# Performance work log

Hardware: AMD Instinct MI355X
Metric: run time of the kernel (lower is better)

The kernel has to match this reference:

```python
import jax, jax.numpy as jnp
import numpy as np

NUM_LEVELS = 16
LEVEL_DIM = 2
LOG2_HASHMAP = 19
TABLE_SIZE = 1 << LOG2_HASHMAP
BASE_RES = 16
PER_LEVEL_SCALE = 2.0
N_QUERIES = 1 << 20

# spatial hashing primes (instant-NGP / Minkowski-style coordinate hash)
_PRIMES = jnp.array([1, 2654435761, 805459861], dtype=jnp.uint32)
# 8 trilinear corner offsets [8,3]
_OFFS = jnp.array([[i, j, k] for i in (0, 1) for j in (0, 1) for k in (0, 1)], dtype=jnp.int32)


def setup_inputs() -> dict:
    key = jax.random.key(0)
    k1, k2 = jax.random.split(key)
    inputs = jax.random.uniform(k1, (N_QUERIES, 3), dtype=jnp.float32, minval=-1.0, maxval=1.0)
    embeddings = jax.random.normal(k2, (NUM_LEVELS, TABLE_SIZE, LEVEL_DIM), dtype=jnp.float32) * 1e-2
    return {"inputs": inputs, "embeddings": embeddings, "bound": 1}


def _encode(inputs, embeddings, bound):
    # channel permutation as in the torch forward: inputs[..., [2, 0, 1]]
    x = inputs[..., jnp.array([2, 0, 1])]
    u = (x / bound + 1.0) * 0.5  # normalize to [0, 1], [N,3]
    resolutions = jnp.asarray(
        np.floor(BASE_RES * PER_LEVEL_SCALE ** np.arange(NUM_LEVELS)), dtype=jnp.float32
    )

    def level_lookup(_, level):
        emb, res = level  # emb [T,F], res scalar
        pos = u * res - 0.5  # align_corners=False
        pos0 = jnp.floor(pos)
        frac = pos - pos0  # [N,3]
        corners = pos0.astype(jnp.int32)[:, None, :] + _OFFS[None]  # [N,8,3]
        cu = corners.astype(jnp.uint32)
        h = (cu[..., 0] * _PRIMES[0]) ^ (cu[..., 1] * _PRIMES[1]) ^ (cu[..., 2] * _PRIMES[2])
        idx = (h & jnp.uint32(TABLE_SIZE - 1)).astype(jnp.int32)  # [N,8]
        feats = emb[idx]  # [N,8,F] gather into sparse grid hash map
        w = jnp.prod(
            jnp.where(_OFFS[None].astype(bool), frac[:, None, :], 1.0 - frac[:, None, :]),
            axis=-1,
        )  # [N,8] trilinear weights
        return None, jnp.sum(feats * w[..., None], axis=1)  # [N,F]

    _, per_level = jax.lax.scan(level_lookup, None, (embeddings, resolutions))  # [L,N,F]
    N = inputs.shape[0]
    # concat per-level features along last dim (level-major), matching torch.cat
    return jnp.moveaxis(per_level, 0, 1).reshape(N, NUM_LEVELS * LEVEL_DIM)


def reference(inputs, embeddings, bound):
    return _encode(inputs, embeddings, float(bound))
```

## Files before the change

### kernel.cpp

```cpp
#include <hip/hip_runtime.h>
#include <hip/hip_fp16.h>

#define NUM_LEVELS 16
#define LOG2_HASHMAP 19
#define TABLE_SIZE (1u << LOG2_HASHMAP)
#define HASH_MASK (TABLE_SIZE - 1u)
#define BASE_RES 16
#define N_QUERIES (1 << 20)
#define BLK 256
#define BLOCKS_PER_LEVEL (N_QUERIES / BLK)

__device__ __forceinline__ float decode_bound(const void* p) {
    int iv = *(const int*)p;
    float fv = __int_as_float(iv);
    float afv = fabsf(fv);
    if (afv >= 1e-8f && afv <= 1e8f) return fv;
    return (float)iv;
}

template <bool USE_WS>
__global__ __launch_bounds__(BLK, 8)
void gather_kernel(const float* __restrict__ in,
                   const float* __restrict__ emb,
                   const void*  __restrict__ bound_ptr,
                   float* __restrict__ dst)
{
    const unsigned P1 = 2654435761u, P2 = 805459861u;
    const int level = blockIdx.x / BLOCKS_PER_LEVEL;
    const int chunk = blockIdx.x % BLOCKS_PER_LEVEL;
    const int n = chunk * BLK + threadIdx.x;

    const float bound = decode_bound(bound_ptr);

    float i0 = in[(size_t)n * 3 + 0];
    float i1 = in[(size_t)n * 3 + 1];
    float i2 = in[(size_t)n * 3 + 2];

    float u0 = __fmul_rn(__fadd_rn(__fdiv_rn(i2, bound), 1.0f), 0.5f);
    float u1 = __fmul_rn(__fadd_rn(__fdiv_rn(i0, bound), 1.0f), 0.5f);
    float u2 = __fmul_rn(__fadd_rn(__fdiv_rn(i1, bound), 1.0f), 0.5f);

    float res = (float)(BASE_RES << level);

    float p0 = __fadd_rn(__fmul_rn(u0, res), -0.5f);
    float p1 = __fadd_rn(__fmul_rn(u1, res), -0.5f);
    float p2 = __fadd_rn(__fmul_rn(u2, res), -0.5f);
    float g0 = floorf(p0), g1 = floorf(p1), g2 = floorf(p2);
    float fr0 = __fsub_rn(p0, g0), fr1 = __fsub_rn(p1, g1), fr2 = __fsub_rn(p2, g2);
    int c0 = (int)g0, c1 = (int)g1, c2 = (int)g2;

    unsigned b0  = (unsigned)c0;
    unsigned b0p = b0 + 1u;
    unsigned b1  = (unsigned)c1 * P1;
    unsigned b1p = b1 + P1;
    unsigned b2  = (unsigned)c2 * P2;
    unsigned b2p = b2 + P2;

    const float2* tbl  = (const float2*)emb + (size_t)level * TABLE_SIZE;
    const float4* tbl4 = (const float4*)tbl;

    unsigned X[4];
    X[0] = b1  ^ b2;
    X[1] = b1  ^ b2p;
    X[2] = b1p ^ b2;
    X[3] = b1p ^ b2p;

    const bool odd = (b0 & 1u) != 0u;

    unsigned E0[4];
    float4 v4[4];
    #pragma unroll
    for (int m = 0; m < 4; ++m) {
        E0[m] = (b0 ^ X[m]) & HASH_MASK;
        v4[m] = tbl4[E0[m] >> 1];
    }

    float2 fb[4] = {make_float2(0.f,0.f), make_float2(0.f,0.f),
                    make_float2(0.f,0.f), make_float2(0.f,0.f)};
    if (odd) {
        #pragma unroll
        for (int m = 0; m < 4; ++m)
            fb[m] = tbl[(b0p ^ X[m]) & HASH_MASK];
    }

    float2 f[8];
    #pragma unroll
    for (int m = 0; m < 4; ++m) {
        bool hi = (E0[m] & 1u) != 0u;
        float2 lo2 = make_float2(v4[m].x, v4[m].y);
        float2 hi2 = make_float2(v4[m].z, v4[m].w);
        f[m]     = hi ? hi2 : lo2;
        f[4 + m] = odd ? fb[m] : (hi ? lo2 : hi2);
    }

    float wx[2] = {1.0f - fr0, fr0};
    float wy[2] = {1.0f - fr1, fr1};
    float wz[2] = {1.0f - fr2, fr2};

    float a0 = 0.0f, a1 = 0.0f;
    #pragma unroll
    for (int c = 0; c < 8; ++c) {
        float w = wx[(c >> 2) & 1] * wy[(c >> 1) & 1] * wz[c & 1];
        a0 += f[c].x * w;
        a1 += f[c].y * w;
    }

    if (USE_WS) {
        __half2 h = __floats2half2_rn(a0, a1);
        union { __half2 h; unsigned u; } cv; cv.h = h;
        unsigned* o = (unsigned*)dst + (size_t)level * N_QUERIES + n;
        *o = cv.u;
    } else {
        float2* o = (float2*)(dst + (size_t)n * 32 + 2 * level);
        *o = make_float2(a0, a1);
    }
}

__global__ __launch_bounds__(BLK, 4)
void transpose_kernel(const unsigned* __restrict__ ws, float* __restrict__ out)
{
    __shared__ unsigned s[NUM_LEVELS][BLK + 1];
    const int n0 = blockIdx.x * BLK;

    #pragma unroll
    for (int l = 0; l < NUM_LEVELS; ++l) {
        s[l][threadIdx.x] = ws[(size_t)l * N_QUERIES + n0 + threadIdx.x];
    }
    __syncthreads();

    float4* o = (float4*)out + (size_t)n0 * 8;
    #pragma unroll
    for (int r = 0; r < 8; ++r) {
        int t = r * BLK + (int)threadIdx.x;
        int n = t >> 3;
        int q = t & 7;
        union { unsigned u; __half2 h; } ca, cb;
        ca.u = s[2 * q][n];
        cb.u = s[2 * q + 1][n];
        float2 a = __half22float2(ca.h);
        float2 b = __half22float2(cb.h);
        o[t] = make_float4(a.x, a.y, b.x, b.y);
    }
}

extern "C" void kernel_launch(void* const* d_in, const int* in_sizes, int n_in,
                              void* d_out, int out_size, void* d_ws, size_t ws_size,
                              hipStream_t stream) {
    const float* in   = (const float*)d_in[0];
    const float* emb  = (const float*)d_in[1];
    const void*  bptr = d_in[2];
    float* out = (float*)d_out;

    const size_t need = (size_t)N_QUERIES * NUM_LEVELS * sizeof(unsigned);
    dim3 block(BLK);
    dim3 ggrid(NUM_LEVELS * BLOCKS_PER_LEVEL);

    if (ws_size >= need) {
        float* ws = (float*)d_ws;
        gather_kernel<true><<<ggrid, block, 0, stream>>>(in, emb, bptr, ws);
        transpose_kernel<<<N_QUERIES / BLK, block, 0, stream>>>((const unsigned*)ws, out);
    } else {
        gather_kernel<false><<<ggrid, block, 0, stream>>>(in, emb, bptr, out);
    }
}
```

Measured before the change: 623.6 us.

## Fuse per-level gather and transpose into one kernel looping over levels

Replaces the level-major gather kernel plus shared-memory transpose with a single kernel where each thread loops over all 16 levels and stages half-precision results in shared memory before writing the interleaved output. This removes the workspace round trip and the second launch. In exchange, the concurrently accessed embedding working set grows from one level's table to all levels, which may reduce L2 hit rates, and the grid shrinks to one block per 256 queries with serialized levels per thread.

```diff
diff --git a/kernel.cpp b/kernel.cpp
--- a/kernel.cpp
+++ b/kernel.cpp
@@ -8,7 +8,7 @@
 #define BASE_RES 16
 #define N_QUERIES (1 << 20)
 #define BLK 256
-#define BLOCKS_PER_LEVEL (N_QUERIES / BLK)
+#define NBLOCKS (N_QUERIES / BLK)
 
 __device__ __forceinline__ float decode_bound(const void* p) {
     int iv = *(const int*)p;
@@ -18,17 +18,14 @@
     return (float)iv;
 }
 
-template <bool USE_WS>
 __global__ __launch_bounds__(BLK, 8)
-void gather_kernel(const float* __restrict__ in,
-                   const float* __restrict__ emb,
-                   const void*  __restrict__ bound_ptr,
-                   float* __restrict__ dst)
+void fused_kernel(const float* __restrict__ in,
+                  const float* __restrict__ emb,
+                  const void*  __restrict__ bound_ptr,
+                  float* __restrict__ out)
 {
     const unsigned P1 = 2654435761u, P2 = 805459861u;
-    const int level = blockIdx.x / BLOCKS_PER_LEVEL;
-    const int chunk = blockIdx.x % BLOCKS_PER_LEVEL;
-    const int n = chunk * BLK + threadIdx.x;
+    const int n = blockIdx.x * BLK + threadIdx.x;
 
     const float bound = decode_bound(bound_ptr);
 
@@ -40,103 +37,91 @@
     float u1 = __fmul_rn(__fadd_rn(__fdiv_rn(i0, bound), 1.0f), 0.5f);
     float u2 = __fmul_rn(__fadd_rn(__fdiv_rn(i1, bound), 1.0f), 0.5f);
 
-    float res = (float)(BASE_RES << level);
+    __shared__ unsigned s[BLK][NUM_LEVELS + 1];
 
-    float p0 = __fadd_rn(__fmul_rn(u0, res), -0.5f);
-    float p1 = __fadd_rn(__fmul_rn(u1, res), -0.5f);
-    float p2 = __fadd_rn(__fmul_rn(u2, res), -0.5f);
-    float g0 = floorf(p0), g1 = floorf(p1), g2 = floorf(p2);
-    float fr0 = __fsub_rn(p0, g0), fr1 = __fsub_rn(p1, g1), fr2 = __fsub_rn(p2, g2);
-    int c0 = (int)g0, c1 = (int)g1, c2 = (int)g2;
+    #pragma unroll 1
+    for (int level = 0; level < NUM_LEVELS; ++level) {
+        float res = (float)(BASE_RES << level);
 
-    unsigned b0  = (unsigned)c0;
-    unsigned b0p = b0 + 1u;
-    unsigned b1  = (unsigned)c1 * P1;
-    unsigned b1p = b1 + P1;
-    unsigned b2  = (unsigned)c2 * P2;
-    unsigned b2p = b2 + P2;
+        float p0 = __fadd_rn(__fmul_rn(u0, res), -0.5f);
+        float p1 = __fadd_rn(__fmul_rn(u1, res), -0.5f);
+        float p2 = __fadd_rn(__fmul_rn(u2, res), -0.5f);
+        float g0 = floorf(p0), g1 = floorf(p1), g2 = floorf(p2);
+        float fr0 = __fsub_rn(p0, g0), fr1 = __fsub_rn(p1, g1), fr2 = __fsub_rn(p2, g2);
+        int c0 = (int)g0, c1 = (int)g1, c2 = (int)g2;
 
-    const float2* tbl  = (const float2*)emb + (size_t)level * TABLE_SIZE;
-    const float4* tbl4 = (const float4*)tbl;
+        unsigned b0  = (unsigned)c0;
+        unsigned b0p = b0 + 1u;
+        unsigned b1  = (unsigned)c1 * P1;
+        unsigned b1p = b1 + P1;
+        unsigned b2  = (unsigned)c2 * P2;
+        unsigned b2p = b2 + P2;
 
-    unsigned X[4];
-    X[0] = b1  ^ b2;
-    X[1] = b1  ^ b2p;
-    X[2] = b1p ^ b2;
-    X[3] = b1p ^ b2p;
+        const float2* tbl  = (const float2*)emb + (size_t)level * TABLE_SIZE;
+        const float4* tbl4 = (const float4*)tbl;
 
-    const bool odd = (b0 & 1u) != 0u;
+        unsigned X[4];
+        X[0] = b1  ^ b2;
+        X[1] = b1  ^ b2p;
+        X[2] = b1p ^ b2;
+        X[3] = b1p ^ b2p;
 
-    unsigned E0[4];
-    float4 v4[4];
-    #pragma unroll
-    for (int m = 0; m < 4; ++m) {
-        E0[m] = (b0 ^ X[m]) & HASH_MASK;
-        v4[m] = tbl4[E0[m] >> 1];
+        const bool odd = (b0 & 1u) != 0u;
+
+        unsigned E0[4];
+        float4 v4[4];
+        #pragma unroll
+        for (int m = 0; m < 4; ++m) {
+            E0[m] = (b0 ^ X[m]) & HASH_MASK;
+            v4[m] = tbl4[E0[m] >> 1];
+        }
+
+        float2 fb[4] = {make_float2(0.f,0.f), make_float2(0.f,0.f),
+                        make_float2(0.f,0.f), make_float2(0.f,0.f)};
+        if (odd) {
+            #pragma unroll
+            for (int m = 0; m < 4; ++m)
+                fb[m] = tbl[(b0p ^ X[m]) & HASH_MASK];
+        }
+
+        float2 f[8];
+        #pragma unroll
+        for (int m = 0; m < 4; ++m) {
+            bool hi = (E0[m] & 1u) != 0u;
+            float2 lo2 = make_float2(v4[m].x, v4[m].y);
+            float2 hi2 = make_float2(v4[m].z, v4[m].w);
+            f[m]     = hi ? hi2 : lo2;
+            f[4 + m] = odd ? fb[m] : (hi ? lo2 : hi2);
+        }
+
+        float wx[2] = {1.0f - fr0, fr0};
+        float wy[2] = {1.0f - fr1, fr1};
+        float wz[2] = {1.0f - fr2, fr2};
+
+        float a0 = 0.0f, a1 = 0.0f;
+        #pragma unroll
+        for (int c = 0; c < 8; ++c) {
+            float w = wx[(c >> 2) & 1] * wy[(c >> 1) & 1] * wz[c & 1];
+            a0 += f[c].x * w;
+            a1 += f[c].y * w;
+        }
+
+        __half2 h = __floats2half2_rn(a0, a1);
+        union { __half2 h; unsigned u; } cv; cv.h = h;
+        s[threadIdx.x][level] = cv.u;
     }
 
-    float2 fb[4] = {make_float2(0.f,0.f), make_float2(0.f,0.f),
-                    make_float2(0.f,0.f), make_float2(0.f,0.f)};
-    if (odd) {
-        #pragma unroll
-        for (int m = 0; m < 4; ++m)
-            fb[m] = tbl[(b0p ^ X[m]) & HASH_MASK];
-    }
-
-    float2 f[8];
-    #pragma unroll
-    for (int m = 0; m < 4; ++m) {
-        bool hi = (E0[m] & 1u) != 0u;
-        float2 lo2 = make_float2(v4[m].x, v4[m].y);
-        float2 hi2 = make_float2(v4[m].z, v4[m].w);
-        f[m]     = hi ? hi2 : lo2;
-        f[4 + m] = odd ? fb[m] : (hi ? lo2 : hi2);
-    }
-
-    float wx[2] = {1.0f - fr0, fr0};
-    float wy[2] = {1.0f - fr1, fr1};
-    float wz[2] = {1.0f - fr2, fr2};
-
-    float a0 = 0.0f, a1 = 0.0f;
-    #pragma unroll
-    for (int c = 0; c < 8; ++c) {
-        float w = wx[(c >> 2) & 1] * wy[(c >> 1) & 1] * wz[c & 1];
-        a0 += f[c].x * w;
-        a1 += f[c].y * w;
-    }
-
-    if (USE_WS) {
-        __half2 h = __floats2half2_rn(a0, a1);
-        union { __half2 h; unsigned u; } cv; cv.h = h;
-        unsigned* o = (unsigned*)dst + (size_t)level * N_QUERIES + n;
-        *o = cv.u;
-    } else {
-        float2* o = (float2*)(dst + (size_t)n * 32 + 2 * level);
-        *o = make_float2(a0, a1);
-    }
-}
-
-__global__ __launch_bounds__(BLK, 4)
-void transpose_kernel(const unsigned* __restrict__ ws, float* __restrict__ out)
-{
-    __shared__ unsigned s[NUM_LEVELS][BLK + 1];
-    const int n0 = blockIdx.x * BLK;
-
-    #pragma unroll
-    for (int l = 0; l < NUM_LEVELS; ++l) {
-        s[l][threadIdx.x] = ws[(size_t)l * N_QUERIES + n0 + threadIdx.x];
-    }
     __syncthreads();
 
-    float4* o = (float4*)out + (size_t)n0 * 8;
+    float4* o = (float4*)out + (size_t)blockIdx.x * (BLK * 8);
     #pragma unroll
     for (int r = 0; r < 8; ++r) {
         int t = r * BLK + (int)threadIdx.x;
-        int n = t >> 3;
+        int nl = t >> 3;
         int q = t & 7;
         union { unsigned u; __half2 h; } ca, cb;
-        ca.u = s[2 * q][n];
-        cb.u = s[2 * q + 1][n];
+        ca.u = s[nl][2 * q];
+        cb.u = s[nl][2 * q + 1];
         float2 a = __half22float2(ca.h);
         float2 b = __half22float2(cb.h);
         o[t] = make_float4(a.x, a.y, b.x, b.y);
@@ -151,15 +136,5 @@
     const void*  bptr = d_in[2];
     float* out = (float*)d_out;
 
-    const size_t need = (size_t)N_QUERIES * NUM_LEVELS * sizeof(unsigned);
-    dim3 block(BLK);
-    dim3 ggrid(NUM_LEVELS * BLOCKS_PER_LEVEL);
-
-    if (ws_size >= need) {
-        float* ws = (float*)d_ws;
-        gather_kernel<true><<<ggrid, block, 0, stream>>>(in, emb, bptr, ws);
-        transpose_kernel<<<N_QUERIES / BLK, block, 0, stream>>>((const unsigned*)ws, out);
-    } else {
-        gather_kernel<false><<<ggrid, block, 0, stream>>>(in, emb, bptr, out);
-    }
+    fused_kernel<<<NBLOCKS, BLK, 0, stream>>>(in, emb, bptr, out);
 }
```

Measured after the change: 1.040 ms. 66.8% more time.
